# Performance work log

Hardware: AMD Instinct MI355X
Metric: run time of the kernel (lower is better)

Reference implementation:

```python
import jax, jax.numpy as jnp
import numpy as np

G, N, C_IN, C_OUT, HEADS = 64, 2048, 64, 64, 2
E = 1_000_000
T = G * N  # total flattened nodes
NEG_SLOPE = 0.2  # PyG GATv2Conv default


def setup_inputs() -> dict:
    key = jax.random.key(0)
    k_x, k_e, k_wl, k_wr, k_a, k_b = jax.random.split(key, 6)
    x = jax.random.normal(k_x, (G, N, C_IN), dtype=jnp.float32)
    edge_index = jax.random.randint(k_e, (2, E), 0, T, dtype=jnp.int64)
    # GATv2Conv params (share_weights=False): separate lin_l / lin_r, per-head att vector, bias
    s = 1.0 / np.sqrt(C_IN)
    W_l = jax.random.uniform(k_wl, (C_IN, HEADS * C_OUT), minval=-s, maxval=s, dtype=jnp.float32)
    W_r = jax.random.uniform(k_wr, (C_IN, HEADS * C_OUT), minval=-s, maxval=s, dtype=jnp.float32)
    att = jax.random.normal(k_a, (HEADS, C_OUT), dtype=jnp.float32) * 0.1
    bias = jax.random.normal(k_b, (HEADS * C_OUT,), dtype=jnp.float32) * 0.01
    return {"x": x, "edge_index": edge_index, "W_l": W_l, "W_r": W_r, "att": att, "bias": bias}


def reference(x, edge_index, W_l, W_r, att, bias):
    # Flatten batched nodes: (G, N, C_in) -> (T, C_in)
    x_flat = x.reshape(-1, C_IN)
    # Linear projections per side, split heads: (T, H, C)
    xl = (x_flat @ W_l).reshape(T, HEADS, C_OUT)
    xr = (x_flat @ W_r).reshape(T, HEADS, C_OUT)
    # add_self_loops=True: append (i, i) for every flattened node
    loop = jnp.arange(T, dtype=edge_index.dtype)
    src = jnp.concatenate([edge_index[0], loop])
    dst = jnp.concatenate([edge_index[1], loop])
    # GATv2 scoring: e_ij = att . LeakyReLU(xl[j] + xr[i])  -> (E', H)
    h = jax.nn.leaky_relu(xl[src] + xr[dst], negative_slope=NEG_SLOPE)
    score = jnp.einsum('ehc,hc->eh', h, att)
    # Segment softmax over incoming edges of each destination node
    m = jax.ops.segment_max(score, dst, num_segments=T)  # (T, H)
    ealpha = jnp.exp(score - m[dst])
    denom = jax.ops.segment_sum(ealpha, dst, num_segments=T)
    alpha = ealpha / denom[dst]  # self-loops guarantee denom > 0
    # Scatter-aggregate messages: out[i] = sum_j alpha_ij * xl[j]
    out = jax.ops.segment_sum(alpha[:, :, None] * xl[src], dst, num_segments=T)  # (T, H, C)
    out = out.reshape(T, HEADS * C_OUT) + bias
    return out.reshape(G, N, HEADS * C_OUT)
```

## Files before the change

kernel.cpp:

```cpp
#include <hip/hip_runtime.h>
#include <hip/hip_bf16.h>

#define T_NODES (64 * 2048)
#define CIN 64
#define HC 128
#define NEG_SLOPE 0.2f
#define GEMM_BLOCKS (T_NODES / 64)

typedef unsigned short ushort_t;
typedef __attribute__((ext_vector_type(8))) short bf16x8;
typedef __attribute__((ext_vector_type(4))) float f32x4;
typedef __attribute__((ext_vector_type(2))) float f32x2;

__device__ __forceinline__ ushort_t f2bf(float x) {
    unsigned u = __float_as_uint(x);
    u += 0x7fffu + ((u >> 16) & 1u);
    return (ushort_t)(u >> 16);
}
__device__ __forceinline__ float bf2f(ushort_t b) {
    return __uint_as_float(((unsigned)b) << 16);
}
__device__ __forceinline__ f32x2 bf2x2(unsigned w) {
    f32x2 r;
    r.x = __uint_as_float(w << 16);
    r.y = __uint_as_float(w & 0xffff0000u);
    return r;
}
__device__ __forceinline__ f32x2 pkmax(f32x2 a, f32x2 b) {
    f32x2 r; r.x = fmaxf(a.x, b.x); r.y = fmaxf(a.y, b.y); return r;
}

__global__ __launch_bounds__(256) void prep_init(const float* __restrict__ Wl,
                                                 const float* __restrict__ Wr,
                                                 uint4* __restrict__ wt,
                                                 unsigned* __restrict__ counts,
                                                 unsigned* __restrict__ partials) {
    const int bid = blockIdx.x, tid = threadIdx.x;
    if (bid < 8) {
        const int t = bid * 256 + tid;
        const int n = t & 255, cc = t >> 8;
        const float* Wsrc = ((n < HC) ? Wl : Wr) + (n & (HC - 1));
        union { ushort_t u[8]; uint4 v; } pk;
#pragma unroll
        for (int j = 0; j < 8; ++j) pk.u[j] = f2bf(Wsrc[(cc * 8 + j) * HC]);
        const int sw = (n & 7) << 4;
        *(uint4*)((char*)wt + n * 128 + ((cc * 16) ^ sw)) = pk.v;
        if (bid == 0 && tid < 128) partials[tid] = 0u;
    } else {
        const int i = (bid - 8) * 256 + tid;
        uint4* c4 = (uint4*)counts;
        c4[i * 2]     = (uint4){0, 0, 0, 0};
        c4[i * 2 + 1] = (uint4){0, 0, 0, 0};
    }
}

__global__ __launch_bounds__(256) void gemm_hist(const float* __restrict__ x,
                                                 const uint4* __restrict__ wt,
                                                 ushort_t* __restrict__ xl,
                                                 ushort_t* __restrict__ xr,
                                                 const int* __restrict__ ei,
                                                 unsigned* __restrict__ counts,
                                                 ushort_t* __restrict__ rank,
                                                 int E, int ET, int histBlocks) {
    __shared__ uint4 lds4[2560];
    const int tid = threadIdx.x;

    if (blockIdx.x < histBlocks) {
        const int b = blockIdx.x;
#pragma unroll
        for (int e = 0; e < 4; ++e) {
            int i = b * 1024 + e * 256 + tid;
            if (i < ET) {
                int dst = (i < E) ? ei[E + i] : (i - E);
                rank[i] = (ushort_t)atomicAdd(&counts[dst], 1u);
            }
        }
        return;
    }

    char* abase = (char*)lds4;
    char* wbase = (char*)lds4 + 8192;
    const int row0 = (blockIdx.x - histBlocks) * 64;

    {
        const int r = tid >> 2, c4 = tid & 3;
        const float4* xp = (const float4*)(x + (size_t)(row0 + r) * CIN + c4 * 16);
        float4 f0 = xp[0], f1 = xp[1], f2 = xp[2], f3 = xp[3];
        union { ushort_t u[16]; uint4 v[2]; } pk;
        const float s[16] = {f0.x,f0.y,f0.z,f0.w, f1.x,f1.y,f1.z,f1.w,
                             f2.x,f2.y,f2.z,f2.w, f3.x,f3.y,f3.z,f3.w};
#pragma unroll
        for (int j = 0; j < 16; ++j) pk.u[j] = f2bf(s[j]);
        const int sw = (r & 7) << 4;
        *(uint4*)(abase + r * 128 + ((c4 * 32)      ^ sw)) = pk.v[0];
        *(uint4*)(abase + r * 128 + ((c4 * 32 + 16) ^ sw)) = pk.v[1];
    }
    {
#pragma unroll
        for (int q = 0; q < 8; ++q)
            lds4[512 + q * 256 + tid] = wt[q * 256 + tid];
    }
    __syncthreads();

    const int wave = tid >> 6;
    const int lane = tid & 63;
    const int ar = lane & 15;
    const int kb = lane >> 4;

    bf16x8 afr[2][4], bfr[2][4];
#pragma unroll
    for (int kk = 0; kk < 2; ++kk) {
#pragma unroll
        for (int rt = 0; rt < 4; ++rt) {
            const int r = rt * 16 + ar;
            afr[kk][rt] = *(bf16x8*)(abase + r * 128 + ((kk * 64 + kb * 16) ^ ((r & 7) << 4)));
        }
#pragma unroll
        for (int ct = 0; ct < 4; ++ct) {
            const int n = wave * 64 + ct * 16 + ar;
            bfr[kk][ct] = *(bf16x8*)(wbase + n * 128 + ((kk * 64 + kb * 16) ^ ((n & 7) << 4)));
        }
    }

    f32x4 acc[4][4];
#pragma unroll
    for (int rt = 0; rt < 4; ++rt)
#pragma unroll
        for (int ct = 0; ct < 4; ++ct) acc[rt][ct] = (f32x4){0.f, 0.f, 0.f, 0.f};

#pragma unroll
    for (int kk = 0; kk < 2; ++kk)
#pragma unroll
        for (int rt = 0; rt < 4; ++rt)
#pragma unroll
            for (int ct = 0; ct < 4; ++ct)
                acc[rt][ct] = __builtin_amdgcn_mfma_f32_16x16x32_bf16(
                    afr[kk][rt], bfr[kk][ct], acc[rt][ct], 0, 0, 0);

    ushort_t* op = (wave < 2) ? xl : xr;
    const int colbase = (wave & 1) * 64 + ar;
    const int rowoff = (lane >> 4) * 4;
#pragma unroll
    for (int rt = 0; rt < 4; ++rt)
#pragma unroll
        for (int ct = 0; ct < 4; ++ct)
#pragma unroll
            for (int j = 0; j < 4; ++j)
                op[(size_t)(row0 + rt * 16 + rowoff + j) * HC + colbase + ct * 16] =
                    f2bf(acc[rt][ct][j]);
}

__global__ __launch_bounds__(256) void scan_all(const unsigned* __restrict__ counts,
                                                unsigned* __restrict__ offs,
                                                unsigned* __restrict__ partials) {
    __shared__ unsigned s[256];
    __shared__ unsigned wsum[4];
    const int b = blockIdx.x, t = threadIdx.x;
    const int base_i = b * 1024 + t * 4;
    uint4 c = *(const uint4*)(counts + base_i);
    unsigned mysum = c.x + c.y + c.z + c.w;
    s[t] = mysum;
    __syncthreads();
    for (int off = 1; off < 256; off <<= 1) {
        unsigned v = (t >= off) ? s[t - off] : 0u;
        __syncthreads();
        s[t] += v;
        __syncthreads();
    }
    const unsigned excl = s[t] - mysum;
    if (t == 255)
        __hip_atomic_store(&partials[b], s[255] | 0x80000000u,
                           __ATOMIC_RELEASE, __HIP_MEMORY_SCOPE_AGENT);
    unsigned bs = 0;
    if (t < b) {
        unsigned v;
        do {
            v = __hip_atomic_load(&partials[t], __ATOMIC_ACQUIRE,
                                  __HIP_MEMORY_SCOPE_AGENT);
        } while (!(v & 0x80000000u));
        bs = v & 0x7fffffffu;
    }
#pragma unroll
    for (int off = 32; off; off >>= 1) bs += __shfl_xor(bs, off);
    if ((t & 63) == 0) wsum[t >> 6] = bs;
    __syncthreads();
    const unsigned base = wsum[0] + wsum[1] + wsum[2] + wsum[3];
    uint4 o;
    o.x = excl + base;
    o.y = o.x + c.x;
    o.z = o.y + c.y;
    o.w = o.z + c.z;
    *(uint4*)(offs + base_i) = o;
}

__global__ void scatter_edges(const int* __restrict__ ei,
                              const unsigned* __restrict__ offs,
                              const ushort_t* __restrict__ rank,
                              int* __restrict__ sorted_src, int E, int ET) {
    int i = blockIdx.x * 256 + threadIdx.x;
    if (i >= ET) return;
    int src, dst;
    if (i < E) { src = ei[i]; dst = ei[E + i]; }
    else       { src = dst = i - E; }
    sorted_src[offs[dst] + rank[i]] = src;
}

__global__ __launch_bounds__(256) void fused_aggr(const ushort_t* __restrict__ xl,
                                                  const ushort_t* __restrict__ xr,
                                                  const int* __restrict__ sorted_src,
                                                  const unsigned* __restrict__ offs,
                                                  const unsigned* __restrict__ counts,
                                                  const float* __restrict__ att,
                                                  const float* __restrict__ bias,
                                                  float* __restrict__ out) {
    const int tid = threadIdx.x;
    const int lane = tid & 63;
    int node = (blockIdx.x * 256 + tid) >> 6;
    node = __builtin_amdgcn_readfirstlane(node);
    const int slot = lane >> 4;
    const int sub  = lane & 15;
    const unsigned cb2 = (unsigned)sub * 16u;

    f32x2 attv[4], xrv[4];
    {
        const f32x2* ap = (const f32x2*)(att + sub * 8);
#pragma unroll
        for (int q = 0; q < 4; ++q) attv[q] = ap[q];
        const uint4 xv = *(const uint4*)((const char*)xr + (((unsigned)node << 8) + cb2));
        const unsigned* xw = (const unsigned*)&xv;
#pragma unroll
        for (int q = 0; q < 4; ++q) xrv[q] = bf2x2(xw[q]);
    }

    const int start = (int)offs[node];
    const int cnt   = (int)counts[node];
    const int rounds = (cnt + 3) >> 2;

    f32x2 acc2[4];
#pragma unroll
    for (int q = 0; q < 4; ++q) acc2[q] = (f32x2){0.f, 0.f};
    float d = 0.f;

    for (int r = 0; r < rounds; ++r) {
        const int k = r * 4 + slot;
        const bool valid = k < cnt;
        const int src = sorted_src[start + (valid ? k : 0)];
        const uint4 v = *(const uint4*)((const char*)xl + (((unsigned)src << 8) + cb2));
        const unsigned* vw = (const unsigned*)&v;
        f32x2 a2[4];
        f32x2 p2 = (f32x2){0.f, 0.f};
#pragma unroll
        for (int q = 0; q < 4; ++q) {
            a2[q] = bf2x2(vw[q]);
            f32x2 z = a2[q] + xrv[q];
            z = pkmax(z, z * NEG_SLOPE);
            p2 += attv[q] * z;
        }
        float p = p2.x + p2.y;
        p += __shfl_xor(p, 1);
        p += __shfl_xor(p, 2);
        p += __shfl_xor(p, 4);
        const float e = valid ? __expf(p) : 0.f;
        d += e;
        const f32x2 ev = (f32x2){e, e};
#pragma unroll
        for (int q = 0; q < 4; ++q) acc2[q] += ev * a2[q];
    }

#pragma unroll
    for (int off = 16; off <= 32; off <<= 1) {
        d += __shfl_xor(d, off);
#pragma unroll
        for (int q = 0; q < 4; ++q) {
            acc2[q].x += __shfl_xor(acc2[q].x, off);
            acc2[q].y += __shfl_xor(acc2[q].y, off);
        }
    }

    if (slot == 0) {
        const float inv = 1.f / d;
        const f32x2* bp = (const f32x2*)(bias + sub * 8);
        float4 o0, o1;
        o0.x = acc2[0].x * inv + bp[0].x; o0.y = acc2[0].y * inv + bp[0].y;
        o0.z = acc2[1].x * inv + bp[1].x; o0.w = acc2[1].y * inv + bp[1].y;
        o1.x = acc2[2].x * inv + bp[2].x; o1.y = acc2[2].y * inv + bp[2].y;
        o1.z = acc2[3].x * inv + bp[3].x; o1.w = acc2[3].y * inv + bp[3].y;
        float* op = out + (size_t)node * HC + sub * 8;
        *(float4*)op = o0;
        *(float4*)(op + 4) = o1;
    }
}

extern "C" void kernel_launch(void* const* d_in, const int* in_sizes, int n_in,
                              void* d_out, int out_size, void* d_ws, size_t ws_size,
                              hipStream_t stream) {
    const float* x    = (const float*)d_in[0];
    const int*   ei   = (const int*)d_in[1];
    const float* Wl   = (const float*)d_in[2];
    const float* Wr   = (const float*)d_in[3];
    const float* att  = (const float*)d_in[4];
    const float* bias = (const float*)d_in[5];
    float* out = (float*)d_out;

    const int E  = in_sizes[1] / 2;
    const int ET = E + T_NODES;

    ushort_t* xl = (ushort_t*)d_ws;
    ushort_t* xr = xl + (size_t)T_NODES * HC;
    int* sorted_src = (int*)(xr + (size_t)T_NODES * HC);
    unsigned* counts   = (unsigned*)(sorted_src + ET);
    unsigned* offs     = counts + T_NODES;
    unsigned* partials = offs + T_NODES;
    ushort_t* rank     = (ushort_t*)(partials + 128);
    uint4* wt          = (uint4*)(rank + ((ET + 7) & ~7));

    prep_init<<<72, 256, 0, stream>>>(Wl, Wr, wt, counts, partials);

    const int histBlocks = (ET + 1023) / 1024;
    gemm_hist<<<histBlocks + GEMM_BLOCKS, 256, 0, stream>>>(x, wt, xl, xr,
                                                            ei, counts, rank,
                                                            E, ET, histBlocks);

    scan_all<<<T_NODES / 1024, 256, 0, stream>>>(counts, offs, partials);
    int eblocks = (ET + 255) / 256;
    scatter_edges<<<eblocks, 256, 0, stream>>>(ei, offs, rank, sorted_src, E, ET);

    fused_aggr<<<T_NODES / 4, 256, 0, stream>>>(xl, xr, sorted_src, offs, counts,
                                                att, bias, out);
}
```

Baseline: 165.1 us.

## Stage GEMM outputs through LDS for coalesced stores; fuse scan with edge scatter

The GEMM epilogue now writes bf16 results into shared memory, then copies full rows out with 16-byte vector stores instead of scattered 2-byte stores. The scan and scatter kernels are merged into one 128-block kernel that uses a global atomic barrier after the scan, then runs a grid-stride loop over edges. This drops one kernel launch and improves store coalescing. In exchange, the scatter phase runs on only 128 blocks, which may limit parallelism, and the barrier depends on all 128 blocks being resident at once.

```diff
diff --git a/kernel.cpp b/kernel.cpp
--- a/kernel.cpp
+++ b/kernel.cpp
@@ -45,7 +45,7 @@
         for (int j = 0; j < 8; ++j) pk.u[j] = f2bf(Wsrc[(cc * 8 + j) * HC]);
         const int sw = (n & 7) << 4;
         *(uint4*)((char*)wt + n * 128 + ((cc * 16) ^ sw)) = pk.v;
-        if (bid == 0 && tid < 128) partials[tid] = 0u;
+        if (bid == 0) partials[tid] = 0u;
     } else {
         const int i = (bid - 8) * 256 + tid;
         uint4* c4 = (uint4*)counts;
@@ -121,6 +121,7 @@
             bfr[kk][ct] = *(bf16x8*)(wbase + n * 128 + ((kk * 64 + kb * 16) ^ ((n & 7) << 4)));
         }
     }
+    __syncthreads();
 
     f32x4 acc[4][4];
 #pragma unroll
@@ -137,22 +138,35 @@
                 acc[rt][ct] = __builtin_amdgcn_mfma_f32_16x16x32_bf16(
                     afr[kk][rt], bfr[kk][ct], acc[rt][ct], 0, 0, 0);
 
-    ushort_t* op = (wave < 2) ? xl : xr;
-    const int colbase = (wave & 1) * 64 + ar;
-    const int rowoff = (lane >> 4) * 4;
+    ushort_t* lh = (ushort_t*)lds4;
+    const int tilecol0 = ((wave >> 1) << 7) + ((wave & 1) << 6) + ar;
 #pragma unroll
     for (int rt = 0; rt < 4; ++rt)
 #pragma unroll
         for (int ct = 0; ct < 4; ++ct)
 #pragma unroll
-            for (int j = 0; j < 4; ++j)
-                op[(size_t)(row0 + rt * 16 + rowoff + j) * HC + colbase + ct * 16] =
-                    f2bf(acc[rt][ct][j]);
-}
-
-__global__ __launch_bounds__(256) void scan_all(const unsigned* __restrict__ counts,
-                                                unsigned* __restrict__ offs,
-                                                unsigned* __restrict__ partials) {
+            for (int j = 0; j < 4; ++j) {
+                const int row = rt * 16 + kb * 4 + j;
+                lh[row * 264 + tilecol0 + ct * 16] = f2bf(acc[rt][ct][j]);
+            }
+    __syncthreads();
+    {
+        const int frow = tid >> 2, q = tid & 3;
+        const uint4* srcv = (const uint4*)(lh + frow * 264 + q * 64);
+        ushort_t* dsta = (q < 2) ? xl : xr;
+        uint4* dstv = (uint4*)(dsta + (size_t)(row0 + frow) * HC + (q & 1) * 64);
+#pragma unroll
+        for (int m = 0; m < 8; ++m) dstv[m] = srcv[m];
+    }
+}
+
+__global__ __launch_bounds__(256) void scan_scatter(const unsigned* __restrict__ counts,
+                                                    unsigned* __restrict__ offs,
+                                                    unsigned* __restrict__ partials,
+                                                    const int* __restrict__ ei,
+                                                    const ushort_t* __restrict__ rank,
+                                                    int* __restrict__ sorted_src,
+                                                    int E, int ET) {
     __shared__ unsigned s[256];
     __shared__ unsigned wsum[4];
     const int b = blockIdx.x, t = threadIdx.x;
@@ -191,18 +205,25 @@
     o.z = o.y + c.y;
     o.w = o.z + c.z;
     *(uint4*)(offs + base_i) = o;
-}
-
-__global__ void scatter_edges(const int* __restrict__ ei,
-                              const unsigned* __restrict__ offs,
-                              const ushort_t* __restrict__ rank,
-                              int* __restrict__ sorted_src, int E, int ET) {
-    int i = blockIdx.x * 256 + threadIdx.x;
-    if (i >= ET) return;
-    int src, dst;
-    if (i < E) { src = ei[i]; dst = ei[E + i]; }
-    else       { src = dst = i - E; }
-    sorted_src[offs[dst] + rank[i]] = src;
+
+    __syncthreads();
+    if (t == 0) {
+        __hip_atomic_fetch_add(&partials[128], 1u, __ATOMIC_ACQ_REL,
+                               __HIP_MEMORY_SCOPE_AGENT);
+        unsigned v;
+        do {
+            v = __hip_atomic_load(&partials[128], __ATOMIC_ACQUIRE,
+                                  __HIP_MEMORY_SCOPE_AGENT);
+        } while (v < 128u);
+    }
+    __syncthreads();
+
+    for (int i = b * 256 + t; i < ET; i += 128 * 256) {
+        int src, dst;
+        if (i < E) { src = ei[i]; dst = ei[E + i]; }
+        else       { src = dst = i - E; }
+        sorted_src[offs[dst] + rank[i]] = src;
+    }
 }
 
 __global__ __launch_bounds__(256) void fused_aggr(const ushort_t* __restrict__ xl,
@@ -311,7 +332,7 @@
     unsigned* counts   = (unsigned*)(sorted_src + ET);
     unsigned* offs     = counts + T_NODES;
     unsigned* partials = offs + T_NODES;
-    ushort_t* rank     = (ushort_t*)(partials + 128);
+    ushort_t* rank     = (ushort_t*)(partials + 256);
     uint4* wt          = (uint4*)(rank + ((ET + 7) & ~7));
 
     prep_init<<<72, 256, 0, stream>>>(Wl, Wr, wt, counts, partials);
@@ -321,9 +342,8 @@
                                                             ei, counts, rank,
                                                             E, ET, histBlocks);
 
-    scan_all<<<T_NODES / 1024, 256, 0, stream>>>(counts, offs, partials);
-    int eblocks = (ET + 255) / 256;
-    scatter_edges<<<eblocks, 256, 0, stream>>>(ei, offs, rank, sorted_src, E, ET);
+    scan_scatter<<<128, 256, 0, stream>>>(counts, offs, partials, ei, rank,
+                                          sorted_src, E, ET);
 
     fused_aggr<<<T_NODES / 4, 256, 0, stream>>>(xl, xr, sorted_src, offs, counts,
                                                 att, bias, out);
```

Result: slower. 190.7 us (+15.5%).
